# Performance work log

Measured on AMD Instinct MI355X. Metric: run time of the kernel, lower is better.

Reference implementation:

```python
import jax, jax.numpy as jnp
import numpy as np

NHEADS = 16


def setup_inputs() -> dict:
    key = jax.random.key(0)
    ks = jax.random.split(key, 5)
    B, S, D = 2, 2048, 1024
    x = jax.random.normal(ks[0], (B, S, D), dtype=jnp.float32)
    W_packed = jax.random.normal(ks[1], (3 * D, D), dtype=jnp.float32) * (1.0 / np.sqrt(D))
    b_packed = jax.random.normal(ks[2], (3 * D,), dtype=jnp.float32) * 0.02
    W_out = jax.random.normal(ks[3], (D, D), dtype=jnp.float32) * (1.0 / np.sqrt(D))
    b_out = jax.random.normal(ks[4], (D,), dtype=jnp.float32) * 0.02
    return {"x": x, "W_packed": W_packed, "b_packed": b_packed, "W_out": W_out, "b_out": b_out}


def reference(x, W_packed, b_packed, W_out, b_out):
    B, S, D = x.shape
    H = NHEADS
    hd = D // H
    # packed QKV projection (self-attention: q is k is v)
    qkv = x @ W_packed.T + b_packed                       # [B,S,3D]
    q, k, v = jnp.split(qkv, 3, axis=-1)

    def heads(t):
        return t.reshape(B, S, H, hd).transpose(0, 2, 1, 3)  # [B,H,S,hd]

    q, k, v = map(heads, (q, k, v))

    # ALiBi slopes per flex path: exp2(-(h+1)*8/H)
    slopes = jnp.exp2(-(jnp.arange(1, H + 1, dtype=x.dtype) * (8.0 / H)))  # [H]
    pos = jnp.arange(S)
    rel = (pos[None, :] - pos[:, None]).astype(x.dtype)    # kv_idx - q_idx, [S,S]
    bias = slopes[:, None, None] * rel                     # [H,S,S]
    causal = pos[None, :] <= pos[:, None]                  # allowed positions
    neg = jnp.finfo(x.dtype).min
    attn_mask = jnp.where(causal[None, :, :], bias, neg)   # [H,S,S]

    scale = 1.0 / np.sqrt(hd)
    scores = jnp.einsum("bhqd,bhkd->bhqk", q, k) * scale + attn_mask[None]
    attn = jax.nn.softmax(scores, axis=-1)
    out = jnp.einsum("bhqk,bhkd->bhqd", attn, v)           # [B,H,S,hd]
    out = out.transpose(0, 2, 1, 3).reshape(B, S, D)
    return out @ W_out.T + b_out
```

## Files before the change

### kernel.cpp

```cpp
#include <hip/hip_runtime.h>

typedef float f32x4 __attribute__((ext_vector_type(4)));
typedef __bf16 bf16x8 __attribute__((ext_vector_type(8)));
typedef unsigned short u16;

__device__ __forceinline__ f32x4 mfma16(bf16x8 a, bf16x8 b, f32x4 c) {
  return __builtin_amdgcn_mfma_f32_16x16x32_bf16(a, b, c, 0, 0, 0);
}

__device__ __forceinline__ void gll16(const void* g, void* l) {
  __builtin_amdgcn_global_load_lds(
      (const __attribute__((address_space(1))) void*)g,
      (__attribute__((address_space(3))) void*)l, 16, 0, 0);
}

__global__ void cvt_kernel(const float* __restrict__ in, __bf16* __restrict__ out, int n8) {
  int idx = blockIdx.x * blockDim.x + threadIdx.x;
  int stride = gridDim.x * blockDim.x;
  for (int i = idx; i < n8; i += stride) {
    const float* p = in + (size_t)i * 8;
    f32x4 a = *(const f32x4*)p;
    f32x4 b = *(const f32x4*)(p + 4);
    bf16x8 r;
#pragma unroll
    for (int j = 0; j < 4; ++j) {
      r[j] = (__bf16)a[j];
      r[4 + j] = (__bf16)b[j];
    }
    *(bf16x8*)(out + (size_t)i * 8) = r;
  }
}

template <int MODE>
__global__ __launch_bounds__(256, 2) void gemm_bt(
    const u16* __restrict__ A, const u16* __restrict__ B,
    const float* __restrict__ bias, float* __restrict__ Cout,
    __bf16* __restrict__ qb, __bf16* __restrict__ kp, __bf16* __restrict__ vp,
    int M, int N, int K) {
  __shared__ u16 lA[128 * 32];
  __shared__ u16 lB[128 * 32];
  const int tid = threadIdx.x;
  const int wid = tid >> 6;
  const int lane = tid & 63;
  const int lr = lane & 15;
  const int lg = lane >> 4;
  const int bm = blockIdx.x * 128;
  const int bn = blockIdx.y * 128;
  const int wm = (wid >> 1) * 64;
  const int wn = (wid & 1) * 64;

  f32x4 acc[4][4] = {};

  for (int kt = 0; kt < K; kt += 32) {
    __syncthreads();
#pragma unroll
    for (int j = 0; j < 2; ++j) {
      int beta = tid * 16 + j * 4096;
      int row = beta >> 6;
      int ce = (beta & 63) >> 1;
      gll16(A + (size_t)(bm + row) * K + kt + ce,
            (char*)lA + (wid << 10) + (j << 12));
      gll16(B + (size_t)(bn + row) * K + kt + ce,
            (char*)lB + (wid << 10) + (j << 12));
    }
    __syncthreads();
    bf16x8 af[4], bfr[4];
#pragma unroll
    for (int mt = 0; mt < 4; ++mt)
      af[mt] = *(const bf16x8*)&lA[(wm + mt * 16 + lr) * 32 + lg * 8];
#pragma unroll
    for (int nt = 0; nt < 4; ++nt)
      bfr[nt] = *(const bf16x8*)&lB[(wn + nt * 16 + lr) * 32 + lg * 8];
#pragma unroll
    for (int mt = 0; mt < 4; ++mt)
#pragma unroll
      for (int nt = 0; nt < 4; ++nt)
        acc[mt][nt] = mfma16(af[mt], bfr[nt], acc[mt][nt]);
  }

#pragma unroll
  for (int nt = 0; nt < 4; ++nt) {
    int col = bn + wn + nt * 16 + lr;
    float bv = bias[col];
#pragma unroll
    for (int mt = 0; mt < 4; ++mt) {
#pragma unroll
      for (int r = 0; r < 4; ++r) {
        int row = bm + wm + mt * 16 + lg * 4 + r;
        float val = acc[mt][nt][r] + bv;
        if (MODE == 0) {
          Cout[(size_t)row * N + col] = val;
        } else {
          __bf16 bx = (__bf16)val;
          int b = row >> 11, s = row & 2047;
          int third = col >> 10, hd = col & 1023;
          int h = hd >> 6, d = hd & 63;
          if (third == 0) {
            qb[(size_t)row * 1024 + hd] = bx;
          } else {
            int bh = b * 16 + h, t = s >> 6, sr = s & 63;
            size_t tb = ((size_t)(bh * 32 + t)) * 4096;
            if (third == 1)
              kp[tb + (sr >> 4) * 1024 + (d >> 5) * 512 + ((d >> 3) & 3) * 128 +
                 (sr & 15) * 8 + (d & 7)] = bx;
            else
              vp[tb + (d >> 4) * 1024 + (sr >> 5) * 512 + ((sr >> 3) & 3) * 128 +
                 (d & 15) * 8 + (sr & 7)] = bx;
          }
        }
      }
    }
  }
}

__global__ __launch_bounds__(64, 4) void attn_kernel(
    const __bf16* __restrict__ qb, const __bf16* __restrict__ kp,
    const __bf16* __restrict__ vp, __bf16* __restrict__ aout) {
  __shared__ __bf16 p_lds[16][72];
  const int lane = threadIdx.x & 63;
  const int lr = lane & 15;
  const int lg = lane >> 4;

  const int lid = blockIdx.x;
  const int xcd = lid & 7;
  const int rest = lid >> 3;
  const int bh = xcd * 4 + (rest & 3);
  const int a16 = 127 - (rest >> 2);
  const int b = bh >> 4, h = bh & 15;
  const int qr0 = a16 * 16;
  const int ntl = (a16 >> 2) + 1;

  const float LOG2E = 1.4426950408889634f;
  const float c1 = 0.125f * LOG2E;
  const float c2 = exp2f(-(float)(h + 1) * 0.5f) * LOG2E;

  bf16x8 ones;
#pragma unroll
  for (int j = 0; j < 8; ++j) ones[j] = (__bf16)1.0f;

  const u16* ktiles = (const u16*)kp + (size_t)bh * 32 * 4096;
  const u16* vtiles = (const u16*)vp + (size_t)bh * 32 * 4096;

  const __bf16* qrow = qb + (size_t)(b * 2048 + qr0 + lr) * 1024 + h * 64;
  bf16x8 qf0 = *(const bf16x8*)(qrow + lg * 8);
  bf16x8 qf1 = *(const bf16x8*)(qrow + 32 + lg * 8);

  float m[4], l[4], cq[4];
  f32x4 o[4];
#pragma unroll
  for (int r = 0; r < 4; ++r) {
    m[r] = 0.f;
    l[r] = 0.f;
    cq[r] = c2 * (float)(qr0 + lg * 4 + r);
  }
#pragma unroll
  for (int dt = 0; dt < 4; ++dt) o[dt] = (f32x4){0.f, 0.f, 0.f, 0.f};

  for (int t = 0; t < ntl; ++t) {
    const u16* kb = ktiles + (size_t)t * 4096;
    const u16* vb = vtiles + (size_t)t * 4096;
    const int kv = t * 64;
    const bool last = (t == ntl - 1);

    bf16x8 ka[8], va[8];
#pragma unroll
    for (int j = 0; j < 8; ++j)
      ka[j] = *(const bf16x8*)(kb + j * 512 + lane * 8);
#pragma unroll
    for (int j = 0; j < 8; ++j)
      va[j] = *(const bf16x8*)(vb + j * 512 + lane * 8);

    f32x4 s[4];
#pragma unroll
    for (int nt = 0; nt < 4; ++nt) {
      f32x4 tt = (f32x4){0.f, 0.f, 0.f, 0.f};
      tt = mfma16(qf0, ka[nt * 2], tt);
      tt = mfma16(qf1, ka[nt * 2 + 1], tt);
      s[nt] = tt;
    }

#pragma unroll
    for (int nt = 0; nt < 4; ++nt) {
      float bnt = c2 * (float)(kv + nt * 16 + lr);
#pragma unroll
      for (int r = 0; r < 4; ++r)
        s[nt][r] = __builtin_fmaf(s[nt][r], c1, bnt - cq[r]);
    }
    if (last) {
#pragma unroll
      for (int nt = 0; nt < 4; ++nt) {
        float kf = (float)(kv + nt * 16 + lr);
#pragma unroll
        for (int r = 0; r < 4; ++r) {
          float qi = (float)(qr0 + lg * 4 + r);
          if (kf > qi) s[nt][r] = -1e30f;
        }
      }
    }

    float pm[4];
#pragma unroll
    for (int r = 0; r < 4; ++r)
      pm[r] = fmaxf(fmaxf(s[0][r], s[1][r]), fmaxf(s[2][r], s[3][r]));
    bool ok = (pm[0] <= m[0] + 8.f) && (pm[1] <= m[1] + 8.f) &&
              (pm[2] <= m[2] + 8.f) && (pm[3] <= m[3] + 8.f);
    if (!__all(ok)) {
#pragma unroll
      for (int r = 0; r < 4; ++r)
#pragma unroll
        for (int d = 1; d < 16; d <<= 1)
          pm[r] = fmaxf(pm[r], __shfl_xor(pm[r], d));
#pragma unroll
      for (int r = 0; r < 4; ++r) {
        float mn = fmaxf(m[r], pm[r]);
        float fac = __builtin_amdgcn_exp2f(m[r] - mn);
        m[r] = mn;
        l[r] *= fac;
#pragma unroll
        for (int dt = 0; dt < 4; ++dt) o[dt][r] *= fac;
      }
    }

#pragma unroll
    for (int nt = 0; nt < 4; ++nt)
#pragma unroll
      for (int r = 0; r < 4; ++r) {
        float e = __builtin_amdgcn_exp2f(s[nt][r] - m[r]);
        p_lds[lg * 4 + r][nt * 16 + lr] = (__bf16)e;
      }

    bf16x8 pa0 = *(const bf16x8*)&p_lds[lr][lg * 8];
    bf16x8 pa1 = *(const bf16x8*)&p_lds[lr][32 + lg * 8];

    {
      f32x4 tt = (f32x4){0.f, 0.f, 0.f, 0.f};
      tt = mfma16(pa0, ones, tt);
      tt = mfma16(pa1, ones, tt);
#pragma unroll
      for (int r = 0; r < 4; ++r) l[r] += tt[r];
    }

#pragma unroll
    for (int dt = 0; dt < 4; ++dt) {
      o[dt] = mfma16(pa0, va[dt * 2], o[dt]);
      o[dt] = mfma16(pa1, va[dt * 2 + 1], o[dt]);
    }
  }

#pragma unroll
  for (int dt = 0; dt < 4; ++dt)
#pragma unroll
    for (int r = 0; r < 4; ++r) {
      float val = o[dt][r] / l[r];
      aout[(size_t)(b * 2048 + qr0 + lg * 4 + r) * 1024 + h * 64 + dt * 16 + lr] =
          (__bf16)val;
    }
}

extern "C" void kernel_launch(void* const* d_in, const int* in_sizes, int n_in,
                              void* d_out, int out_size, void* d_ws, size_t ws_size,
                              hipStream_t stream) {
  (void)in_sizes; (void)n_in; (void)out_size; (void)ws_size;
  const float* x = (const float*)d_in[0];
  const float* Wp = (const float*)d_in[1];
  const float* bp = (const float*)d_in[2];
  const float* Wo = (const float*)d_in[3];
  const float* bo = (const float*)d_in[4];
  float* out = (float*)d_out;

  char* ws = (char*)d_ws;
  u16* xb  = (u16*)(ws);
  u16* wpb = (u16*)(ws + (size_t)(8u << 20));
  u16* wob = (u16*)(ws + (size_t)(14u << 20));
  u16* qbp = (u16*)(ws + (size_t)(16u << 20));
  u16* kpp = (u16*)(ws + (size_t)(24u << 20));
  u16* vpp = (u16*)(ws + (size_t)(32u << 20));
  u16* ab  = xb;

  cvt_kernel<<<2048, 256, 0, stream>>>(x, (__bf16*)xb, 4096 * 1024 / 8);
  cvt_kernel<<<1536, 256, 0, stream>>>(Wp, (__bf16*)wpb, 3072 * 1024 / 8);
  cvt_kernel<<<512, 256, 0, stream>>>(Wo, (__bf16*)wob, 1024 * 1024 / 8);
  gemm_bt<1><<<dim3(32, 24), 256, 0, stream>>>(
      xb, wpb, bp, nullptr, (__bf16*)qbp, (__bf16*)kpp, (__bf16*)vpp,
      4096, 3072, 1024);
  attn_kernel<<<4096, 64, 0, stream>>>(
      (const __bf16*)qbp, (const __bf16*)kpp, (const __bf16*)vpp, (__bf16*)ab);
  gemm_bt<0><<<dim3(32, 8), 256, 0, stream>>>(
      ab, wob, bo, out, nullptr, nullptr, nullptr, 4096, 1024, 1024);
}
```

Measured before the change: 116.3 us.

## Double-buffer GEMM LDS tiles, shrink tiles, and swizzle block order for XCDs

Converts the bf16 GEMM to double-buffered LDS staging, so the next K-slice's global_load_lds is issued before computing on the current one. This replaces the two barriers per iteration with one. Tile sizes become template parameters (128x64 for QKV, 64x64 for the output projection), which raises the block count and the occupancy hint to 4. Blocks are launched on a 1D grid remapped with an XCD-aware swizzle to improve L2 locality. Smaller tiles reduce per-block reuse and raise LDS traffic per FLOP, and it is unclear whether a single barrier guarantees the prefetched loads are complete.

New measurement: 125.3 us. +7.8%, slower.

```diff
diff --git a/kernel.cpp b/kernel.cpp
--- a/kernel.cpp
+++ b/kernel.cpp
@@ -31,59 +31,80 @@
   }
 }
 
-template <int MODE>
-__global__ __launch_bounds__(256, 2) void gemm_bt(
+template <int BM, int BN, int MODE>
+__global__ __launch_bounds__(256, 4) void gemm_bt(
     const u16* __restrict__ A, const u16* __restrict__ B,
     const float* __restrict__ bias, float* __restrict__ Cout,
     __bf16* __restrict__ qb, __bf16* __restrict__ kp, __bf16* __restrict__ vp,
-    int M, int N, int K) {
-  __shared__ u16 lA[128 * 32];
-  __shared__ u16 lB[128 * 32];
+    int M, int N, int K, int mtiles) {
+  constexpr int MREP = BM / 32;
+  constexpr int NREP = BN / 32;
+  constexpr int LA = BM / 64;
+  constexpr int LB = BN / 64;
+  __shared__ u16 lA[2 * BM * 32];
+  __shared__ u16 lB[2 * BN * 32];
   const int tid = threadIdx.x;
   const int wid = tid >> 6;
   const int lane = tid & 63;
   const int lr = lane & 15;
   const int lg = lane >> 4;
-  const int bm = blockIdx.x * 128;
-  const int bn = blockIdx.y * 128;
-  const int wm = (wid >> 1) * 64;
-  const int wn = (wid & 1) * 64;
-
-  f32x4 acc[4][4] = {};
-
+
+  const int nwg = gridDim.x;
+  const int lid = blockIdx.x;
+  const int sw = (lid & 7) * (nwg >> 3) + (lid >> 3);
+  const int bm = (sw % mtiles) * BM;
+  const int bn = (sw / mtiles) * BN;
+
+  const int wm = (wid >> 1) * (BM / 2);
+  const int wn = (wid & 1) * (BN / 2);
+
+  f32x4 acc[MREP][NREP] = {};
+
+  auto stage = [&](int bf, int kt) {
+    char* baseA = (char*)lA + bf * (BM * 64);
+    char* baseB = (char*)lB + bf * (BN * 64);
+#pragma unroll
+    for (int j = 0; j < LA; ++j) {
+      int off = (tid + j * 256) * 16;
+      gll16(A + (size_t)(bm + (off >> 6)) * K + kt + ((off & 63) >> 1),
+            baseA + off);
+    }
+#pragma unroll
+    for (int j = 0; j < LB; ++j) {
+      int off = (tid + j * 256) * 16;
+      gll16(B + (size_t)(bn + (off >> 6)) * K + kt + ((off & 63) >> 1),
+            baseB + off);
+    }
+  };
+
+  int buf = 0;
+  stage(0, 0);
   for (int kt = 0; kt < K; kt += 32) {
     __syncthreads();
-#pragma unroll
-    for (int j = 0; j < 2; ++j) {
-      int beta = tid * 16 + j * 4096;
-      int row = beta >> 6;
-      int ce = (beta & 63) >> 1;
-      gll16(A + (size_t)(bm + row) * K + kt + ce,
-            (char*)lA + (wid << 10) + (j << 12));
-      gll16(B + (size_t)(bn + row) * K + kt + ce,
-            (char*)lB + (wid << 10) + (j << 12));
-    }
-    __syncthreads();
-    bf16x8 af[4], bfr[4];
-#pragma unroll
-    for (int mt = 0; mt < 4; ++mt)
-      af[mt] = *(const bf16x8*)&lA[(wm + mt * 16 + lr) * 32 + lg * 8];
-#pragma unroll
-    for (int nt = 0; nt < 4; ++nt)
-      bfr[nt] = *(const bf16x8*)&lB[(wn + nt * 16 + lr) * 32 + lg * 8];
-#pragma unroll
-    for (int mt = 0; mt < 4; ++mt)
-#pragma unroll
-      for (int nt = 0; nt < 4; ++nt)
+    if (kt + 32 < K) stage(buf ^ 1, kt + 32);
+    const u16* cA = lA + buf * BM * 32;
+    const u16* cB = lB + buf * BN * 32;
+    bf16x8 af[MREP], bfr[NREP];
+#pragma unroll
+    for (int mt = 0; mt < MREP; ++mt)
+      af[mt] = *(const bf16x8*)&cA[(wm + mt * 16 + lr) * 32 + lg * 8];
+#pragma unroll
+    for (int nt = 0; nt < NREP; ++nt)
+      bfr[nt] = *(const bf16x8*)&cB[(wn + nt * 16 + lr) * 32 + lg * 8];
+#pragma unroll
+    for (int mt = 0; mt < MREP; ++mt)
+#pragma unroll
+      for (int nt = 0; nt < NREP; ++nt)
         acc[mt][nt] = mfma16(af[mt], bfr[nt], acc[mt][nt]);
-  }
-
-#pragma unroll
-  for (int nt = 0; nt < 4; ++nt) {
+    buf ^= 1;
+  }
+
+#pragma unroll
+  for (int nt = 0; nt < NREP; ++nt) {
     int col = bn + wn + nt * 16 + lr;
     float bv = bias[col];
 #pragma unroll
-    for (int mt = 0; mt < 4; ++mt) {
+    for (int mt = 0; mt < MREP; ++mt) {
 #pragma unroll
       for (int r = 0; r < 4; ++r) {
         int row = bm + wm + mt * 16 + lg * 4 + r;
@@ -280,11 +301,11 @@
   cvt_kernel<<<2048, 256, 0, stream>>>(x, (__bf16*)xb, 4096 * 1024 / 8);
   cvt_kernel<<<1536, 256, 0, stream>>>(Wp, (__bf16*)wpb, 3072 * 1024 / 8);
   cvt_kernel<<<512, 256, 0, stream>>>(Wo, (__bf16*)wob, 1024 * 1024 / 8);
-  gemm_bt<1><<<dim3(32, 24), 256, 0, stream>>>(
+  gemm_bt<128, 64, 1><<<1536, 256, 0, stream>>>(
       xb, wpb, bp, nullptr, (__bf16*)qbp, (__bf16*)kpp, (__bf16*)vpp,
-      4096, 3072, 1024);
+      4096, 3072, 1024, 32);
   attn_kernel<<<4096, 64, 0, stream>>>(
       (const __bf16*)qbp, (const __bf16*)kpp, (const __bf16*)vpp, (__bf16*)ab);
-  gemm_bt<0><<<dim3(32, 8), 256, 0, stream>>>(
-      ab, wob, bo, out, nullptr, nullptr, nullptr, 4096, 1024, 1024);
-}
+  gemm_bt<64, 64, 0><<<1024, 256, 0, stream>>>(
+      ab, wob, bo, out, nullptr, nullptr, nullptr, 4096, 1024, 1024, 64);
+}
```

## Pre-swizzle GEMM operands into MFMA fragment order and drop LDS staging

Applied to the files above, without the earlier changes.

The fp32-to-bf16 conversion now writes x, W_packed and W_out directly into a fragment-packed layout, and the three conversions are fused into one launch. The attention kernel writes its output in the same packed layout. The GEMMs become single-wave 64x64 tile kernels that load MFMA fragments straight from global memory with register double-buffering and no LDS or barriers. An XCD-aware tile swizzle is also added. This removes LDS traffic and block-level syncs, but each wave now reuses operands less, so global and L2 traffic per tile goes up.

After: 123.6 us. 1.06x slower.

```diff
diff --git a/kernel.cpp b/kernel.cpp
--- a/kernel.cpp
+++ b/kernel.cpp
@@ -8,85 +8,99 @@
   return __builtin_amdgcn_mfma_f32_16x16x32_bf16(a, b, c, 0, 0, 0);
 }
 
-__device__ __forceinline__ void gll16(const void* g, void* l) {
-  __builtin_amdgcn_global_load_lds(
-      (const __attribute__((address_space(1))) void*)g,
-      (__attribute__((address_space(3))) void*)l, 16, 0, 0);
-}
-
-__global__ void cvt_kernel(const float* __restrict__ in, __bf16* __restrict__ out, int n8) {
+__device__ __forceinline__ int pidx16(int row, int kc) {
+  return ((((row >> 6) * 32 + (kc >> 2)) * 4 + ((row >> 4) & 3)) << 6) +
+         ((kc & 3) << 4) + (row & 15);
+}
+
+__global__ void cvt3_kernel(const float* __restrict__ x,
+                            const float* __restrict__ wp,
+                            const float* __restrict__ wo,
+                            u16* __restrict__ apx, u16* __restrict__ bpx,
+                            u16* __restrict__ wox) {
   int idx = blockIdx.x * blockDim.x + threadIdx.x;
   int stride = gridDim.x * blockDim.x;
-  for (int i = idx; i < n8; i += stride) {
-    const float* p = in + (size_t)i * 8;
-    f32x4 a = *(const f32x4*)p;
-    f32x4 b = *(const f32x4*)(p + 4);
+  for (int i = idx; i < 1048576; i += stride) {
+    const float* src;
+    u16* dst;
+    int j;
+    if (i < 524288) {
+      j = i; src = x + (size_t)j * 8; dst = apx;
+    } else if (i < 917504) {
+      j = i - 524288; src = wp + (size_t)j * 8; dst = bpx;
+    } else {
+      j = i - 917504; src = wo + (size_t)j * 8; dst = wox;
+    }
+    f32x4 a = *(const f32x4*)src;
+    f32x4 b = *(const f32x4*)(src + 4);
     bf16x8 r;
 #pragma unroll
-    for (int j = 0; j < 4; ++j) {
-      r[j] = (__bf16)a[j];
-      r[4 + j] = (__bf16)b[j];
-    }
-    *(bf16x8*)(out + (size_t)i * 8) = r;
+    for (int e = 0; e < 4; ++e) {
+      r[e] = (__bf16)a[e];
+      r[4 + e] = (__bf16)b[e];
+    }
+    int row = j >> 7, kc = j & 127;
+    *(bf16x8*)(dst + (size_t)pidx16(row, kc) * 8) = r;
   }
 }
 
 template <int MODE>
-__global__ __launch_bounds__(256, 2) void gemm_bt(
-    const u16* __restrict__ A, const u16* __restrict__ B,
+__global__ __launch_bounds__(64, 3) void gemm_frag(
+    const u16* __restrict__ apx, const u16* __restrict__ bpx,
     const float* __restrict__ bias, float* __restrict__ Cout,
     __bf16* __restrict__ qb, __bf16* __restrict__ kp, __bf16* __restrict__ vp,
-    int M, int N, int K) {
-  __shared__ u16 lA[128 * 32];
-  __shared__ u16 lB[128 * 32];
-  const int tid = threadIdx.x;
-  const int wid = tid >> 6;
-  const int lane = tid & 63;
-  const int lr = lane & 15;
-  const int lg = lane >> 4;
-  const int bm = blockIdx.x * 128;
-  const int bn = blockIdx.y * 128;
-  const int wm = (wid >> 1) * 64;
-  const int wn = (wid & 1) * 64;
+    int N, int ntiles) {
+  const int lane = threadIdx.x & 63;
+  const int lr = lane & 15, lg = lane >> 4;
+  const int nwg = gridDim.x;
+  const int lid = blockIdx.x;
+  const int sw = (lid & 7) * (nwg >> 3) + (lid >> 3);
+  const int ni = sw % ntiles, mi = sw / ntiles;
+
+  const u16* ab = apx + (size_t)mi * 65536 + lane * 8;
+  const u16* bb = bpx + (size_t)ni * 65536 + lane * 8;
 
   f32x4 acc[4][4] = {};
-
-  for (int kt = 0; kt < K; kt += 32) {
-    __syncthreads();
-#pragma unroll
-    for (int j = 0; j < 2; ++j) {
-      int beta = tid * 16 + j * 4096;
-      int row = beta >> 6;
-      int ce = (beta & 63) >> 1;
-      gll16(A + (size_t)(bm + row) * K + kt + ce,
-            (char*)lA + (wid << 10) + (j << 12));
-      gll16(B + (size_t)(bn + row) * K + kt + ce,
-            (char*)lB + (wid << 10) + (j << 12));
-    }
-    __syncthreads();
-    bf16x8 af[4], bfr[4];
+  bf16x8 a0[4], b0[4], a1[4], b1[4];
+#pragma unroll
+  for (int mt = 0; mt < 4; ++mt) {
+    a0[mt] = *(const bf16x8*)(ab + mt * 512);
+    b0[mt] = *(const bf16x8*)(bb + mt * 512);
+  }
+  for (int kt = 0; kt < 32; kt += 2) {
+#pragma unroll
+    for (int mt = 0; mt < 4; ++mt) {
+      a1[mt] = *(const bf16x8*)(ab + (kt + 1) * 2048 + mt * 512);
+      b1[mt] = *(const bf16x8*)(bb + (kt + 1) * 2048 + mt * 512);
+    }
 #pragma unroll
     for (int mt = 0; mt < 4; ++mt)
-      af[mt] = *(const bf16x8*)&lA[(wm + mt * 16 + lr) * 32 + lg * 8];
-#pragma unroll
-    for (int nt = 0; nt < 4; ++nt)
-      bfr[nt] = *(const bf16x8*)&lB[(wn + nt * 16 + lr) * 32 + lg * 8];
+#pragma unroll
+      for (int nt = 0; nt < 4; ++nt)
+        acc[mt][nt] = mfma16(a0[mt], b0[nt], acc[mt][nt]);
+    if (kt + 2 < 32) {
+#pragma unroll
+      for (int mt = 0; mt < 4; ++mt) {
+        a0[mt] = *(const bf16x8*)(ab + (kt + 2) * 2048 + mt * 512);
+        b0[mt] = *(const bf16x8*)(bb + (kt + 2) * 2048 + mt * 512);
+      }
+    }
 #pragma unroll
     for (int mt = 0; mt < 4; ++mt)
 #pragma unroll
       for (int nt = 0; nt < 4; ++nt)
-        acc[mt][nt] = mfma16(af[mt], bfr[nt], acc[mt][nt]);
+        acc[mt][nt] = mfma16(a1[mt], b1[nt], acc[mt][nt]);
   }
 
 #pragma unroll
   for (int nt = 0; nt < 4; ++nt) {
-    int col = bn + wn + nt * 16 + lr;
+    int col = ni * 64 + nt * 16 + lr;
     float bv = bias[col];
 #pragma unroll
     for (int mt = 0; mt < 4; ++mt) {
 #pragma unroll
       for (int r = 0; r < 4; ++r) {
-        int row = bm + wm + mt * 16 + lg * 4 + r;
+        int row = mi * 64 + mt * 16 + lg * 4 + r;
         float val = acc[mt][nt][r] + bv;
         if (MODE == 0) {
           Cout[(size_t)row * N + col] = val;
@@ -98,8 +112,8 @@
           if (third == 0) {
             qb[(size_t)row * 1024 + hd] = bx;
           } else {
-            int bh = b * 16 + h, t = s >> 6, sr = s & 63;
-            size_t tb = ((size_t)(bh * 32 + t)) * 4096;
+            int bh = b * 16 + h, t2 = s >> 6, sr = s & 63;
+            size_t tb = ((size_t)(bh * 32 + t2)) * 4096;
             if (third == 1)
               kp[tb + (sr >> 4) * 1024 + (d >> 5) * 512 + ((d >> 3) & 3) * 128 +
                  (sr & 15) * 8 + (d & 7)] = bx;
@@ -115,7 +129,7 @@
 
 __global__ __launch_bounds__(64, 4) void attn_kernel(
     const __bf16* __restrict__ qb, const __bf16* __restrict__ kp,
-    const __bf16* __restrict__ vp, __bf16* __restrict__ aout) {
+    const __bf16* __restrict__ vp, u16* __restrict__ abp) {
   __shared__ __bf16 p_lds[16][72];
   const int lane = threadIdx.x & 63;
   const int lr = lane & 15;
@@ -247,13 +261,16 @@
     }
   }
 
+  const int mi_g = b * 32 + (a16 >> 2);
 #pragma unroll
   for (int dt = 0; dt < 4; ++dt)
 #pragma unroll
     for (int r = 0; r < 4; ++r) {
       float val = o[dt][r] / l[r];
-      aout[(size_t)(b * 2048 + qr0 + lg * 4 + r) * 1024 + h * 64 + dt * 16 + lr] =
-          (__bf16)val;
+      __bf16 bx = (__bf16)val;
+      int off16 = (((mi_g * 32 + h * 2 + (dt >> 1)) * 4 + (a16 & 3)) << 6) +
+                  (((dt & 1) * 2 + (lr >> 3)) << 4) + lg * 4 + r;
+      abp[(size_t)off16 * 8 + (lr & 7)] = *(u16*)&bx;
     }
 }
 
@@ -269,22 +286,20 @@
   float* out = (float*)d_out;
 
   char* ws = (char*)d_ws;
-  u16* xb  = (u16*)(ws);
-  u16* wpb = (u16*)(ws + (size_t)(8u << 20));
-  u16* wob = (u16*)(ws + (size_t)(14u << 20));
+  u16* apx = (u16*)(ws);
+  u16* bpx = (u16*)(ws + (size_t)(8u << 20));
+  u16* wox = (u16*)(ws + (size_t)(14u << 20));
   u16* qbp = (u16*)(ws + (size_t)(16u << 20));
   u16* kpp = (u16*)(ws + (size_t)(24u << 20));
   u16* vpp = (u16*)(ws + (size_t)(32u << 20));
-  u16* ab  = xb;
-
-  cvt_kernel<<<2048, 256, 0, stream>>>(x, (__bf16*)xb, 4096 * 1024 / 8);
-  cvt_kernel<<<1536, 256, 0, stream>>>(Wp, (__bf16*)wpb, 3072 * 1024 / 8);
-  cvt_kernel<<<512, 256, 0, stream>>>(Wo, (__bf16*)wob, 1024 * 1024 / 8);
-  gemm_bt<1><<<dim3(32, 24), 256, 0, stream>>>(
-      xb, wpb, bp, nullptr, (__bf16*)qbp, (__bf16*)kpp, (__bf16*)vpp,
-      4096, 3072, 1024);
+  u16* abp = (u16*)(ws + (size_t)(40u << 20));
+
+  cvt3_kernel<<<2048, 256, 0, stream>>>(x, Wp, Wo, apx, bpx, wox);
+  gemm_frag<1><<<3072, 64, 0, stream>>>(
+      apx, bpx, bp, nullptr, (__bf16*)qbp, (__bf16*)kpp, (__bf16*)vpp,
+      3072, 48);
   attn_kernel<<<4096, 64, 0, stream>>>(
-      (const __bf16*)qbp, (const __bf16*)kpp, (const __bf16*)vpp, (__bf16*)ab);
-  gemm_bt<0><<<dim3(32, 8), 256, 0, stream>>>(
-      ab, wob, bo, out, nullptr, nullptr, nullptr, 4096, 1024, 1024);
-}
+      (const __bf16*)qbp, (const __bf16*)kpp, (const __bf16*)vpp, abp);
+  gemm_frag<0><<<1024, 64, 0, stream>>>(
+      abp, wox, bo, out, nullptr, nullptr, nullptr, 1024, 16);
+}
```
